# Optimization experiments

Measured on AMD Instinct MI355X. Metric: run time of the kernel, lower is better.

Reference implementation:

```python
import jax, jax.numpy as jnp
import numpy as np

# dims
B, L, D = 2, 2048, 768
K, KQ, M = 12, 6, 4          # heads, query heads, thetas
H = D // K                    # 64 head dim (expand_factor=1)
NREP = K // KQ                # 2
MEM = K * H                   # 768
FLAT = K * H * M              # 3072
EXP = H * 3                   # 192 (out_expand_factor=3)
DSW = EXP * 2                 # 384 swiglu per head
LAT = D // 4                  # 192
CK = 4                        # conv kernel size
TH_MIN, TH_MAX = 1e-3, 3.0


def setup_inputs() -> dict:
    key = jax.random.key(0)
    ks = jax.random.split(key, 10)
    rn = lambda k, sh, s=0.02: jax.random.normal(k, sh, jnp.float32) * s
    # faithful parameter inits from the flax module
    grid_m = np.geomspace(TH_MIN, TH_MAX, M)
    theta_d_raw = jnp.asarray(
        np.log(np.exp(np.tile(grid_m.reshape(1, 1, 1, 1, M), (1, 1, K, H, 1))) - 1.0 + 1e-4),
        jnp.float32)
    decay_slopes = jnp.asarray(np.log(np.exp(np.geomspace(1e-3, 0.1, K)) - 1.0), jnp.float32)
    return {
        "x": jax.random.normal(ks[0], (B, L, D), jnp.float32),
        "W_mem": rn(ks[1], (D, MEM + K)),
        "conv_k": rn(ks[2], (CK, 1, MEM + K), 0.2),
        "W_q": rn(ks[3], (D, KQ * H * M * 2)),
        "theta_d_raw": theta_d_raw,
        "decay_slopes": decay_slopes,
        "score_scale": jnp.ones((K,), jnp.float32),
        "tanh_scale": jnp.ones((K,), jnp.float32),
        "W_re": rn(ks[4], (K, H, DSW), 0.05),
        "W_im": rn(ks[5], (K, H, DSW), 0.05),
        "norm_scale": jnp.ones((1, 1, K, H), jnp.float32),
        "gate_W": jnp.zeros((D, K), jnp.float32),
        "gate_b": jnp.full((K,), -3.0, jnp.float32),
        "skip_down_W": rn(ks[6], (D, LAT)),
        "skip_up_W": rn(ks[7], (LAT, K * DSW)),
        "highway_scale": jnp.ones((1, 1, K, 1), jnp.float32),
        "out_W": rn(ks[8], (K * EXP, D)),
    }


def reference(x, W_mem, conv_k, W_q, theta_d_raw, decay_slopes, score_scale, tanh_scale,
              W_re, W_im, norm_scale, gate_W, gate_b, skip_down_W, skip_up_W,
              highway_scale, out_W):
    b, l, _ = x.shape
    # memory stream: dense proj + depthwise causal conv
    z = x @ W_mem                                                     # (b,l,MEM+K)
    z = jax.lax.conv_general_dilated(z, conv_k, (1,), [(CK - 1, 0)],
                                     dimension_numbers=('NWC', 'WIO', 'NWC'),
                                     feature_group_count=MEM + K)
    k_val = z[..., :MEM].reshape(b, l, K, H)
    s_raw = z[..., MEM:].reshape(b, l, K, 1)
    q = (x @ W_q).reshape(b, l, KQ, H, M, 2)
    q_re, q_im = q[..., 0], q[..., 1]
    # multi-frequency theta grid + trapezoid quadrature weights
    theta_d = jax.nn.softplus(theta_d_raw) + 1e-4
    ta = jnp.cumsum(theta_d, axis=-1)
    total = ta[..., -1:]
    rng = TH_MAX - TH_MIN
    theta = TH_MIN + ta / total * rng                                 # (1,1,K,H,M)
    dth = (ta[..., 1:] - ta[..., :-1]) * (rng / total)
    w_int = jnp.concatenate([dth[..., :1] * 0.5,
                             0.5 * (dth[..., :-1] + dth[..., 1:]),
                             dth[..., -1:] * 0.5], axis=-1)           # (1,1,K,H,M)
    # ALiBi-like decay anchored at sequence end (all decay heads)
    pos = jnp.arange(l, dtype=jnp.float32)
    slopes = jax.nn.softplus(decay_slopes).reshape(1, 1, K, 1)
    dist = jnp.maximum(jnp.float32(l - 1) - pos, 0.0)
    log_tw = -slopes * dist[None, :, None, None]                      # (1,l,K,1)
    log_p = jnp.clip(score_scale[None, None, :, None] * s_raw, -20.0, 20.0)
    p_w = jnp.exp(log_p + log_tw)                                     # (b,l,K,1)
    # complex rotation of keys by per-head/per-freq phase
    kvw = k_val[..., None] * p_w[..., None]                           # (b,l,K,H,1)
    phi = jnp.tanh(tanh_scale.reshape(1, 1, K, 1, 1) * k_val[..., None]) * theta  # (b,l,K,H,M)
    re_k = kvw * jnp.cos(phi)
    im_k = kvw * jnp.sin(phi)
    # fused prefix-sum over time of (denominator, Re, Im)
    merged = jnp.concatenate([p_w[..., 0],
                              re_k.reshape(b, l, FLAT),
                              im_k.reshape(b, l, FLAT)], axis=-1)
    cs = jnp.cumsum(merged, axis=1)
    den, num_re, num_im = cs[..., :K], cs[..., K:K + FLAT], cs[..., K + FLAT:]
    inv_den = 1.0 / jnp.maximum(den[..., None], 1e-4)                 # (b,l,K,1)
    s_re = (num_re.reshape(b, l, K, H, M) * inv_den[..., None]).reshape(b, l, KQ, NREP, H, M)
    s_im = (num_im.reshape(b, l, K, H, M) * inv_den[..., None]).reshape(b, l, KQ, NREP, H, M)
    w_g = w_int.reshape(1, 1, KQ, NREP, H, M)
    qr, qi = q_re[:, :, :, None], q_im[:, :, :, None]                 # GQA broadcast over n_rep
    out_re = jnp.sum((s_re * qr + s_im * qi) * w_g, axis=-1).reshape(b, l, K, H)
    out_im = jnp.sum((s_im * qr - s_re * qi) * w_g, axis=-1).reshape(b, l, K, H)
    # gated spectral output + low-rank highway skip, swiglu, out proj
    gate = jax.nn.sigmoid(x @ gate_W + gate_b)[..., None]             # (b,l,K,1)
    y_re = jnp.einsum('blkh,khn->blkn', out_re * norm_scale, W_re)
    y_im = jnp.einsum('blkh,khn->blkn', out_im * norm_scale, W_im)
    y_spec = (y_re + y_im) * gate                                     # (b,l,K,DSW)
    y_dir = ((x @ skip_down_W) @ skip_up_W).reshape(b, l, K, DSW)
    yv_s, yg_s = jnp.split(y_spec, 2, axis=-1)
    yv_d, yg_d = jnp.split(y_dir, 2, axis=-1)
    y_val = yv_s + yv_d * highway_scale
    y_gate = yg_s + yg_d * highway_scale
    y = (y_val * jax.nn.silu(y_gate)).reshape(b, l, K * EXP)
    return y @ out_W
```

## Files before the change

kernel.cpp:

```cpp
#include <hip/hip_runtime.h>
#include <math.h>

#define B_    2
#define L_    2048
#define D_    768
#define K_    12
#define KQ_   6
#define M_    4
#define H_    64
#define ZC_   780
#define NTOK_ 4096
#define NC_   64
#define LC_   32
#define QST_  3072
#define XPN_  4096
#define ZOFF_ 3276

typedef __attribute__((ext_vector_type(8))) _Float16 half8;
typedef __attribute__((ext_vector_type(4))) float f32x4;

__device__ __forceinline__ float softplus_f(float x) {
  return (x > 20.f) ? x : log1pf(expf(x));
}

__device__ __forceinline__ float fast_tanh(float x) {
  float xx = fminf(fmaxf(x, -10.f), 10.f);
  float e = __expf(2.f * xx);
  return (e - 1.f) / (e + 1.f);
}

__device__ __forceinline__ void async16(const _Float16* g, _Float16* l) {
  __builtin_amdgcn_global_load_lds(
      (const __attribute__((address_space(1))) unsigned int*)g,
      (__attribute__((address_space(3))) unsigned int*)l, 16, 0, 0);
}

__device__ __forceinline__ int permcol(int n) {
  int isg = (n >= 192) ? 1 : 0;
  int j = n - 192 * isg;
  return (j >> 4) * 32 + (isg << 4) + (j & 15);
}

#define FENCE() asm volatile("" ::: "memory")

__device__ __forceinline__ void cvt_t_body(float (*tile)[33], int bx, int by, int kz,
                                           const float* src, long sKs, int srs,
                                           _Float16* dh, long dKs, int dst, int doff,
                                           int R, int Nact, int Nst, bool perm, float scale) {
  const float* s = src + (size_t)kz * sKs;
  _Float16* dhh = dh + (size_t)kz * dKs;
  const int kb = bx * 32;
  const int nb = by * 32;
  const int tx = threadIdx.x & 31, ty = threadIdx.x >> 5;
  for (int i = ty; i < 32; i += 8) {
    int kk = kb + i, n = nb + tx;
    tile[i][tx] = (kk < R && n < Nact) ? s[(size_t)kk * srs + n] : 0.f;
  }
  __syncthreads();
  for (int i = ty; i < 32; i += 8) {
    int n = nb + i, kk = kb + tx;
    if (kk < R && n < Nst) {
      float v = tile[tx][i] * scale;
      int dn = perm ? permcol(n) : n;
      dhh[(size_t)dn * dst + doff + kk] = (_Float16)v;
    }
  }
}

__global__ __launch_bounds__(256)
void prep_kernel(const float* __restrict__ x,
                 const float* __restrict__ W_mem, const float* __restrict__ W_q,
                 const float* __restrict__ skip_down_W, const float* __restrict__ out_W,
                 const float* __restrict__ W_re, const float* __restrict__ W_im,
                 const float* __restrict__ skip_up_W, const float* __restrict__ hs,
                 const float* __restrict__ gate_W,
                 const float* __restrict__ theta_d_raw, const float* __restrict__ decay,
                 _Float16* __restrict__ x_h,
                 _Float16* __restrict__ xpb_h, _Float16* __restrict__ outw_h,
                 _Float16* __restrict__ bsp_h,
                 float* __restrict__ theta_tab, float* __restrict__ w_tab,
                 float* __restrict__ slopes_sp) {
  __shared__ float tile[32][33];
  int b = blockIdx.x;
  if (b < 3) {
    int idx = b * 256 + threadIdx.x;
    if (idx < K_) slopes_sp[idx] = softplus_f(decay[idx]);
    if (idx >= K_ * H_) return;
    float td[M_], ta[M_];
#pragma unroll
    for (int m = 0; m < M_; ++m) td[m] = softplus_f(theta_d_raw[idx * M_ + m]) + 1e-4f;
    ta[0] = td[0];
#pragma unroll
    for (int m = 1; m < M_; ++m) ta[m] = ta[m - 1] + td[m];
    float total = ta[M_ - 1];
    float rs = 2.999f / total;
#pragma unroll
    for (int m = 0; m < M_; ++m) theta_tab[idx * M_ + m] = 0.001f + ta[m] * rs;
    float d0 = (ta[1] - ta[0]) * rs;
    float d1 = (ta[2] - ta[1]) * rs;
    float d2 = (ta[3] - ta[2]) * rs;
    w_tab[idx * M_ + 0] = 0.5f * d0;
    w_tab[idx * M_ + 1] = 0.5f * (d0 + d1);
    w_tab[idx * M_ + 2] = 0.5f * (d1 + d2);
    w_tab[idx * M_ + 3] = 0.5f * d2;
    return;
  }
  b -= 3;
  if (b < 6360) {
    if (b < 672) {
      cvt_t_body(tile, b % 24, b / 24, 0, W_mem, 0, ZC_, xpb_h + (size_t)ZOFF_ * 768,
                 0, 768, 0, 768, ZC_, ZC_, false, 1.f);
      return;
    }
    b -= 672;
    if (b < 2304) {
      cvt_t_body(tile, b % 24, b / 24, 0, W_q, 0, 3072, xpb_h, 0, 768, 0, 768,
                 3072, 3072, false, 1.f);
      return;
    }
    b -= 2304;
    if (b < 192) {
      cvt_t_body(tile, b % 24, b / 24, 0, skip_down_W, 0, 192, xpb_h + (size_t)3072 * 768,
                 0, 768, 0, 768, 192, 192, false, 1.f);
      return;
    }
    b -= 192;
    if (b < 1728) {
      cvt_t_body(tile, b % 72, b / 72, 0, out_W, 0, 768, outw_h, 0, 2304, 0, 2304,
                 768, 768, false, 1.f);
      return;
    }
    b -= 1728;
    if (b < 288) {
      cvt_t_body(tile, b % 2, (b / 2) % 12, b / 24, W_re, 64L * 384, 384, bsp_h,
                 384L * 320, 320, 0, 64, 384, 384, true, 1.f);
      return;
    }
    b -= 288;
    if (b < 288) {
      cvt_t_body(tile, b % 2, (b / 2) % 12, b / 24, W_im, 64L * 384, 384, bsp_h,
                 384L * 320, 320, 64, 64, 384, 384, true, 1.f);
      return;
    }
    b -= 288;
    if (b < 864) {
      int kz = b / 72;
      cvt_t_body(tile, b % 6, (b / 6) % 12, kz, skip_up_W, 384, 4608, bsp_h,
                 384L * 320, 320, 128, 192, 384, 384, true, hs[kz]);
      return;
    }
    b -= 864;
    cvt_t_body(tile, b, 0, 0, gate_W, 0, K_, xpb_h + (size_t)3264 * 768,
               0, 768, 0, 768, K_, K_, false, 1.f);
    return;
  }
  b -= 6360;
  size_t i = (size_t)b * 256 + threadIdx.x;
  if (i < (size_t)NTOK_ * D_) {
    x_h[i] = (_Float16)x[i];
  }
}

__global__ __launch_bounds__(512, 2)
void xproj256_kernel(const _Float16* __restrict__ Ah, const _Float16* __restrict__ Bh,
                     float* __restrict__ C, _Float16* __restrict__ YH,
                     _Float16* __restrict__ QH, float* __restrict__ GL) {
  __shared__ __align__(16) _Float16 sA[2][2][2][128][32];
  __shared__ __align__(16) _Float16 sB[2][2][2][128][32];

  const int bid = blockIdx.x;
  const int xcd = bid & 7, s = bid >> 3;
  const int by = xcd * 2 + (s & 1);
  const int bx = s >> 1;
  const int bm0 = by * 256, bn0 = bx * 256;

  const int tid = threadIdx.x;
  const int lane = tid & 63;
  const int wave = tid >> 6;
  const int m16 = lane & 15, quad = lane >> 4;
  const int wr = wave >> 2;
  const int wc = wave & 3;
  const int bhalf = wc >> 1;
  const int brow0 = (wc & 1) * 64;

  f32x4 acc[8][4];
#pragma unroll
  for (int i = 0; i < 8; ++i)
#pragma unroll
    for (int j = 0; j < 4; ++j) acc[i][j] = (f32x4){0.f, 0.f, 0.f, 0.f};

  const int sr = tid >> 2;
  const int lb = tid & 3;
  const int ssw = (sr >> 1) & 3;

  auto stageA = [&](int t, int h) {
    const int bb = t & 1;
    const _Float16* g = Ah + (size_t)(bm0 + h * 128 + sr) * 768 + t * 64
                        + ((lb ^ ssw) << 3);
    async16(g,      &sA[bb][h][0][0][0] + (size_t)tid * 8);
    async16(g + 32, &sA[bb][h][1][0][0] + (size_t)tid * 8);
  };
  auto stageB = [&](int t, int h) {
    const int bb = t & 1;
    const _Float16* g = Bh + (size_t)(bn0 + h * 128 + sr) * 768 + t * 64
                        + ((lb ^ ssw) << 3);
    async16(g,      &sB[bb][h][0][0][0] + (size_t)tid * 8);
    async16(g + 32, &sB[bb][h][1][0][0] + (size_t)tid * 8);
  };

  auto ldA = [&](int bb, int r, int kk) -> half8 {
    return *(const half8*)&sA[bb][wr][kk][r][(quad ^ ((r >> 1) & 3)) << 3];
  };
  auto ldB = [&](int bb, int r, int kk) -> half8 {
    return *(const half8*)&sB[bb][bhalf][kk][r][(quad ^ ((r >> 1) & 3)) << 3];
  };

  half8 aLo[8], aHi[8], bLo[4], bHi[4];

  stageB(0, 0); stageB(0, 1); stageA(0, 0); stageA(0, 1);
  stageB(1, 0); stageB(1, 1); stageA(1, 0); stageA(1, 1);
  __builtin_amdgcn_s_waitcnt(0x0F78);
  FENCE(); __builtin_amdgcn_s_barrier(); FENCE();
#pragma unroll
  for (int m = 0; m < 4; ++m)
#pragma unroll
    for (int kk = 0; kk < 2; ++kk) aLo[m * 2 + kk] = ldA(0, m * 16 + m16, kk);
#pragma unroll
  for (int n = 0; n < 2; ++n)
#pragma unroll
    for (int kk = 0; kk < 2; ++kk) bLo[n * 2 + kk] = ldB(0, brow0 + n * 16 + m16, kk);

  for (int t = 0; t < 12; ++t) {
    const int bb = t & 1;
    const int nb = bb ^ 1;
#pragma unroll
    for (int n = 0; n < 2; ++n)
#pragma unroll
      for (int kk = 0; kk < 2; ++kk)
        bHi[n * 2 + kk] = ldB(bb, brow0 + (n + 2) * 16 + m16, kk);
#pragma unroll
    for (int m = 0; m < 4; ++m)
#pragma unroll
      for (int kk = 0; kk < 2; ++kk)
        aHi[m * 2 + kk] = ldA(bb, 64 + m * 16 + m16, kk);
    FENCE(); __builtin_amdgcn_s_barrier(); FENCE();
    if (t < 10) { stageB(t + 2, 0); stageB(t + 2, 1); stageA(t + 2, 0); stageA(t + 2, 1); }
    FENCE();
    if (t < 10)
      __builtin_amdgcn_s_waitcnt(0x0F78);
    else
      __builtin_amdgcn_s_waitcnt(0x0F70);
    FENCE(); __builtin_amdgcn_s_barrier(); FENCE();
    __builtin_amdgcn_s_setprio(1);
#pragma unroll
    for (int kk = 0; kk < 2; ++kk)
#pragma unroll
      for (int m = 0; m < 4; ++m)
#pragma unroll
        for (int n = 0; n < 2; ++n)
          acc[m][n] = __builtin_amdgcn_mfma_f32_16x16x32_f16(aLo[m * 2 + kk], bLo[n * 2 + kk],
                                                             acc[m][n], 0, 0, 0);
#pragma unroll
    for (int kk = 0; kk < 2; ++kk)
#pragma unroll
      for (int m = 0; m < 4; ++m)
#pragma unroll
        for (int n = 2; n < 4; ++n)
          acc[m][n] = __builtin_amdgcn_mfma_f32_16x16x32_f16(aLo[m * 2 + kk], bHi[(n - 2) * 2 + kk],
                                                             acc[m][n], 0, 0, 0);
    __builtin_amdgcn_s_setprio(0);
    if (t < 11) {
#pragma unroll
      for (int m = 0; m < 4; ++m)
#pragma unroll
        for (int kk = 0; kk < 2; ++kk)
          aLo[m * 2 + kk] = ldA(nb, m * 16 + m16, kk);
    }
    __builtin_amdgcn_s_setprio(1);
#pragma unroll
    for (int kk = 0; kk < 2; ++kk)
#pragma unroll
      for (int m = 0; m < 4; ++m)
#pragma unroll
        for (int n = 0; n < 2; ++n)
          acc[m + 4][n] = __builtin_amdgcn_mfma_f32_16x16x32_f16(aHi[m * 2 + kk], bLo[n * 2 + kk],
                                                                 acc[m + 4][n], 0, 0, 0);
    __builtin_amdgcn_s_setprio(0);
    if (t < 11) {
#pragma unroll
      for (int n = 0; n < 2; ++n)
#pragma unroll
        for (int kk = 0; kk < 2; ++kk)
          bLo[n * 2 + kk] = ldB(nb, brow0 + n * 16 + m16, kk);
    }
    __builtin_amdgcn_s_setprio(1);
#pragma unroll
    for (int kk = 0; kk < 2; ++kk)
#pragma unroll
      for (int m = 0; m < 4; ++m)
#pragma unroll
        for (int n = 2; n < 4; ++n)
          acc[m + 4][n] = __builtin_amdgcn_mfma_f32_16x16x32_f16(aHi[m * 2 + kk], bHi[(n - 2) * 2 + kk],
                                                                 acc[m + 4][n], 0, 0, 0);
    __builtin_amdgcn_s_setprio(0);
  }

#pragma unroll
  for (int m = 0; m < 8; ++m) {
    const int row0 = bm0 + wr * 128 + m * 16 + quad * 4;
#pragma unroll
    for (int n = 0; n < 4; ++n) {
      const int col = bn0 + wc * 64 + n * 16 + m16;
      if (col < 3072) {
#pragma unroll
        for (int r = 0; r < 4; ++r)
          QH[(size_t)(row0 + r) * QST_ + col] = (_Float16)acc[m][n][r];
      } else if (col < 3264) {
        const int jj = col - 3072;
#pragma unroll
        for (int r = 0; r < 4; ++r)
          YH[(size_t)(row0 + r) * 192 + jj] = (_Float16)acc[m][n][r];
      } else if (col < 3276) {
        const int kk = col - 3264;
#pragma unroll
        for (int r = 0; r < 4; ++r)
          GL[(size_t)(row0 + r) * K_ + kk] = acc[m][n][r];
      } else if (col < 3276 + ZC_) {
        const int wz = col - ZOFF_;
#pragma unroll
        for (int r = 0; r < 4; ++r)
          C[(size_t)(row0 + r) * ZC_ + wz] = acc[m][n][r];
      }
    }
  }
}

__global__ __launch_bounds__(512, 2)
void outproj256_kernel(const _Float16* __restrict__ Ah, const _Float16* __restrict__ Bh,
                       float* __restrict__ out, float* __restrict__ part) {
  __shared__ __align__(16) _Float16 sA[2][2][2][128][32];
  __shared__ __align__(16) _Float16 sB[2][2][2][128][32];

  const int bid = blockIdx.x;
  const int xcd = bid & 7, s = bid >> 3;
  const int g = xcd * 24 + s;
  const int by = g & 15;
  const int c = g >> 4;
  const int kz_ = c / 3, bx = c - kz_ * 3;
  const int bm0 = by * 256, bn0 = bx * 256;
  const int kt0 = kz_ * 9;

  const int tid = threadIdx.x;
  const int lane = tid & 63;
  const int wave = tid >> 6;
  const int m16 = lane & 15, quad = lane >> 4;
  const int wr = wave >> 2;
  const int wc = wave & 3;
  const int bhalf = wc >> 1;
  const int brow0 = (wc & 1) * 64;

  f32x4 acc[8][4];
#pragma unroll
  for (int i = 0; i < 8; ++i)
#pragma unroll
    for (int j = 0; j < 4; ++j) acc[i][j] = (f32x4){0.f, 0.f, 0.f, 0.f};

  const int sr = tid >> 2;
  const int lbk = tid & 3;
  const int ssw = (sr >> 1) & 3;

  auto stageA = [&](int lt, int h) {
    const int bb = lt & 1;
    const _Float16* gp = Ah + (size_t)(bm0 + h * 128 + sr) * 2304 + (kt0 + lt) * 64
                         + ((lbk ^ ssw) << 3);
    async16(gp,      &sA[bb][h][0][0][0] + (size_t)tid * 8);
    async16(gp + 32, &sA[bb][h][1][0][0] + (size_t)tid * 8);
  };
  auto stageB = [&](int lt, int h) {
    const int bb = lt & 1;
    const _Float16* gp = Bh + (size_t)(bn0 + h * 128 + sr) * 2304 + (kt0 + lt) * 64
                         + ((lbk ^ ssw) << 3);
    async16(gp,      &sB[bb][h][0][0][0] + (size_t)tid * 8);
    async16(gp + 32, &sB[bb][h][1][0][0] + (size_t)tid * 8);
  };

  auto ldA = [&](int bb, int r, int kk) -> half8 {
    return *(const half8*)&sA[bb][wr][kk][r][(quad ^ ((r >> 1) & 3)) << 3];
  };
  auto ldB = [&](int bb, int r, int kk) -> half8 {
    return *(const half8*)&sB[bb][bhalf][kk][r][(quad ^ ((r >> 1) & 3)) << 3];
  };

  half8 aLo[8], aHi[8], bLo[4], bHi[4];

  stageB(0, 0); stageB(0, 1); stageA(0, 0); stageA(0, 1);
  stageB(1, 0); stageB(1, 1); stageA(1, 0); stageA(1, 1);
  __builtin_amdgcn_s_waitcnt(0x0F78);
  FENCE(); __builtin_amdgcn_s_barrier(); FENCE();
#pragma unroll
  for (int m = 0; m < 4; ++m)
#pragma unroll
    for (int kk = 0; kk < 2; ++kk) aLo[m * 2 + kk] = ldA(0, m * 16 + m16, kk);
#pragma unroll
  for (int n = 0; n < 2; ++n)
#pragma unroll
    for (int kk = 0; kk < 2; ++kk) bLo[n * 2 + kk] = ldB(0, brow0 + n * 16 + m16, kk);

  for (int t = 0; t < 9; ++t) {
    const int bb = t & 1;
    const int nb = bb ^ 1;
#pragma unroll
    for (int n = 0; n < 2; ++n)
#pragma unroll
      for (int kk = 0; kk < 2; ++kk)
        bHi[n * 2 + kk] = ldB(bb, brow0 + (n + 2) * 16 + m16, kk);
#pragma unroll
    for (int m = 0; m < 4; ++m)
#pragma unroll
      for (int kk = 0; kk < 2; ++kk)
        aHi[m * 2 + kk] = ldA(bb, 64 + m * 16 + m16, kk);
    FENCE(); __builtin_amdgcn_s_barrier(); FENCE();
    if (t < 7) { stageB(t + 2, 0); stageB(t + 2, 1); stageA(t + 2, 0); stageA(t + 2, 1); }
    FENCE();
    if (t < 7)
      __builtin_amdgcn_s_waitcnt(0x0F78);
    else
      __builtin_amdgcn_s_waitcnt(0x0F70);
    FENCE(); __builtin_amdgcn_s_barrier(); FENCE();
    __builtin_amdgcn_s_setprio(1);
#pragma unroll
    for (int kk = 0; kk < 2; ++kk)
#pragma unroll
      for (int m = 0; m < 4; ++m)
#pragma unroll
        for (int n = 0; n < 2; ++n)
          acc[m][n] = __builtin_amdgcn_mfma_f32_16x16x32_f16(aLo[m * 2 + kk], bLo[n * 2 + kk],
                                                             acc[m][n], 0, 0, 0);
#pragma unroll
    for (int kk = 0; kk < 2; ++kk)
#pragma unroll
      for (int m = 0; m < 4; ++m)
#pragma unroll
        for (int n = 2; n < 4; ++n)
          acc[m][n] = __builtin_amdgcn_mfma_f32_16x16x32_f16(aLo[m * 2 + kk], bHi[(n - 2) * 2 + kk],
                                                             acc[m][n], 0, 0, 0);
    __builtin_amdgcn_s_setprio(0);
    if (t < 8) {
#pragma unroll
      for (int m = 0; m < 4; ++m)
#pragma unroll
        for (int kk = 0; kk < 2; ++kk)
          aLo[m * 2 + kk] = ldA(nb, m * 16 + m16, kk);
    }
    __builtin_amdgcn_s_setprio(1);
#pragma unroll
    for (int kk = 0; kk < 2; ++kk)
#pragma unroll
      for (int m = 0; m < 4; ++m)
#pragma unroll
        for (int n = 0; n < 2; ++n)
          acc[m + 4][n] = __builtin_amdgcn_mfma_f32_16x16x32_f16(aHi[m * 2 + kk], bLo[n * 2 + kk],
                                                                 acc[m + 4][n], 0, 0, 0);
    __builtin_amdgcn_s_setprio(0);
    if (t < 8) {
#pragma unroll
      for (int n = 0; n < 2; ++n)
#pragma unroll
        for (int kk = 0; kk < 2; ++kk)
          bLo[n * 2 + kk] = ldB(nb, brow0 + n * 16 + m16, kk);
    }
    __builtin_amdgcn_s_setprio(1);
#pragma unroll
    for (int kk = 0; kk < 2; ++kk)
#pragma unroll
      for (int m = 0; m < 4; ++m)
#pragma unroll
        for (int n = 2; n < 4; ++n)
          acc[m + 4][n] = __builtin_amdgcn_mfma_f32_16x16x32_f16(aHi[m * 2 + kk], bHi[(n - 2) * 2 + kk],
                                                                 acc[m + 4][n], 0, 0, 0);
    __builtin_amdgcn_s_setprio(0);
  }

  float* dst = (kz_ == 0) ? out : part + (size_t)(kz_ - 1) * NTOK_ * 768;
#pragma unroll
  for (int m = 0; m < 8; ++m) {
    const int row0 = bm0 + wr * 128 + m * 16 + quad * 4;
#pragma unroll
    for (int n = 0; n < 4; ++n) {
      const int col = bn0 + wc * 64 + n * 16 + m16;
#pragma unroll
      for (int r = 0; r < 4; ++r)
        dst[(size_t)(row0 + r) * 768 + col] = acc[m][n][r];
    }
  }
}

__global__ __launch_bounds__(256)
void redout_kernel(float* __restrict__ o, const float* __restrict__ p) {
  const size_t i = (size_t)blockIdx.x * 256 + threadIdx.x;
  const f32x4* pv = (const f32x4*)p;
  f32x4 v = ((const f32x4*)o)[i];
  v += pv[i];
  v += pv[i + 786432];
  v += pv[i + 2 * 786432];
  ((f32x4*)o)[i] = v;
}

__global__ __launch_bounds__(256)
void spec_gemm_kernel(const _Float16* __restrict__ Ah, const _Float16* __restrict__ Bh,
                      const _Float16* __restrict__ A2, _Float16* __restrict__ YH) {
  __shared__ __align__(16) _Float16 sA[2][128 * 32];
  __shared__ __align__(16) _Float16 sB[2][128 * 32];
  const int Kd = 320;
  int bid = blockIdx.x;
  int xcd = bid & 7, s = bid >> 3;
  int kz = s / 12;
  int w = s % 12;
  int bx = w % 3;
  int by = (xcd << 2) + w / 3;
  const _Float16* A0 = Ah + (size_t)kz * ((size_t)NTOK_ * 128);
  const _Float16* B0 = Bh + (size_t)kz * (384L * 320);
  const int bm0 = by * 128;
  const int bn0 = bx * 128;
  const int tid = threadIdx.x;
  const int wave = tid >> 6, lane = tid & 63;
  const int m16 = lane & 15, quad = lane >> 4;
  const int wr = (wave & 1) * 64, wc = (wave >> 1) * 64;

  f32x4 acc[4][4];
#pragma unroll
  for (int i = 0; i < 4; ++i)
#pragma unroll
    for (int j = 0; j < 4; ++j) acc[i][j] = (f32x4){0.f, 0.f, 0.f, 0.f};

  const int lin = tid * 8;
  const int lrow = lin >> 5;
  const int lblk = (lin >> 3) & 3;
  const int csw = ((lblk ^ ((lrow >> 1) & 3)) << 3);

  auto stage = [&](int k0, int kb) {
    if (k0 < 128) {
      const _Float16* gA = A0 + (size_t)(bm0 + lrow) * 128 + (k0 + csw);
      async16(gA, &sA[kb][lin]);
      async16(gA + (size_t)64 * 128, &sA[kb][lin + 2048]);
    } else {
      const _Float16* gA = A2 + (size_t)(bm0 + lrow) * 192 + (k0 - 128 + csw);
      async16(gA, &sA[kb][lin]);
      async16(gA + (size_t)64 * 192, &sA[kb][lin + 2048]);
    }
    const _Float16* gB = B0 + (size_t)(bn0 + lrow) * Kd + (k0 + csw);
    async16(gB, &sB[kb][lin]);
    async16(gB + (size_t)64 * Kd, &sB[kb][lin + 2048]);
  };

  const int niter = Kd / 32;
  stage(0, 0);
  stage(32, 1);

  for (int it = 0; it < niter; ++it) {
    if (it == niter - 1)
      __builtin_amdgcn_s_waitcnt(0x0F70);
    else
      __builtin_amdgcn_s_waitcnt(0x0F74);
    __builtin_amdgcn_s_barrier();
    asm volatile("" ::: "memory");
    const int kb = it & 1;
    half8 a0[4], b0[4];
#pragma unroll
    for (int i = 0; i < 4; ++i) {
      const int rA = wr + i * 16 + m16;
      a0[i] = *(const half8*)&sA[kb][rA * 32 + ((quad ^ ((rA >> 1) & 3)) << 3)];
    }
#pragma unroll
    for (int j = 0; j < 4; ++j) {
      const int rB = wc + j * 16 + m16;
      b0[j] = *(const half8*)&sB[kb][rB * 32 + ((quad ^ ((rB >> 1) & 3)) << 3)];
    }
#pragma unroll
    for (int i = 0; i < 4; ++i)
#pragma unroll
      for (int j = 0; j < 4; ++j)
        acc[i][j] = __builtin_amdgcn_mfma_f32_16x16x32_f16(a0[i], b0[j], acc[i][j], 0, 0, 0);
    asm volatile("" ::: "memory");
    __builtin_amdgcn_s_barrier();
    asm volatile("" ::: "memory");
    if (it + 2 < niter) stage((it + 2) * 32, kb);
  }

#pragma unroll
  for (int i = 0; i < 4; ++i) {
    const int row0 = bm0 + wr + i * 16 + quad * 4;
#pragma unroll
    for (int j = 0; j < 4; j += 2) {
      const int colv = bn0 + wc + j * 16 + m16;
      const int jout = (colv >> 5) * 16 + m16;
#pragma unroll
      for (int r = 0; r < 4; ++r) {
        float val = acc[i][j][r];
        float gg = acc[i][j + 1][r];
        float sg = gg / (1.f + __expf(-gg));
        YH[(size_t)(row0 + r) * 2304 + kz * 192 + jout] = (_Float16)(val * sg);
      }
    }
  }
}

__global__ __launch_bounds__(256)
void pass_a_kernel(const float* __restrict__ zp,
                   const float* __restrict__ ck,
                   const float* __restrict__ theta_tab,
                   const float* __restrict__ score_scale,
                   const float* __restrict__ tanh_scale,
                   const float* __restrict__ slopes_sp,
                   float* __restrict__ csums) {
  const int c = blockIdx.x, k = blockIdx.y, b = blockIdx.z;
  const int tid = threadIdx.x;
  const int m = tid & 3, h = tid >> 2;
  const int l0 = c * LC_;
  const size_t base = (((size_t)b * K_ + k) * NC_ + c) * 513;

  __shared__ float s_pw[LC_];
  __shared__ float s_kv[LC_][H_];
  __shared__ float s_th[LC_][H_];

  if (tid < 32) {
    const int chs = 768 + k;
    const float ss = score_scale[k], slope = slopes_sp[k];
    float cks[4];
#pragma unroll
    for (int w = 0; w < 4; ++w) cks[w] = ck[w * ZC_ + chs];
    float sraw = 0.f;
#pragma unroll
    for (int j = 0; j < 4; ++j) {
      int lp_ = l0 + tid - 3 + j;
      float zs = (lp_ >= 0) ? zp[((size_t)b * L_ + lp_) * ZC_ + chs] : 0.f;
      sraw += zs * cks[j];
    }
    float lp = fminf(fmaxf(ss * sraw, -20.f), 20.f);
    int l = l0 + tid;
    float pw = __expf(lp - slope * (float)(L_ - 1 - l));
    s_pw[tid] = pw;
    float tot = pw;
    tot += __shfl_xor(tot, 1);
    tot += __shfl_xor(tot, 2);
    tot += __shfl_xor(tot, 4);
    tot += __shfl_xor(tot, 8);
    tot += __shfl_xor(tot, 16);
    if (tid == 0) csums[base] = tot;
  }

  {
    const int hh = tid >> 2, g = tid & 3;
    const int chkh = k * H_ + hh;
    const float ts = tanh_scale[k];
    float ckv[4];
#pragma unroll
    for (int w = 0; w < 4; ++w) ckv[w] = ck[w * ZC_ + chkh];
    const int lbase = l0 + g * 8;
    float z3 = 0.f, z2 = 0.f, z1 = 0.f;
#pragma unroll
    for (int p = 0; p < 3; ++p) {
      int lp_ = lbase - 3 + p;
      if (lp_ >= 0) {
        float z = zp[((size_t)b * L_ + lp_) * ZC_ + chkh];
        if (p == 0) z3 = z; else if (p == 1) z2 = z; else z1 = z;
      }
    }
#pragma unroll
    for (int j = 0; j < 8; ++j) {
      float z0 = zp[((size_t)b * L_ + lbase + j) * ZC_ + chkh];
      float kv = z3 * ckv[0] + z2 * ckv[1] + z1 * ckv[2] + z0 * ckv[3];
      z3 = z2; z2 = z1; z1 = z0;
      s_kv[g * 8 + j][hh] = kv;
      s_th[g * 8 + j][hh] = fast_tanh(ts * kv);
    }
  }
  __syncthreads();

  const int chk = k * H_ + h;
  const float theta_v = theta_tab[chk * M_ + m];
  float sre = 0.f, sim = 0.f;
#pragma unroll 8
  for (int ll = 0; ll < LC_; ++ll) {
    float kvp = s_kv[ll][h] * s_pw[ll];
    float ph = s_th[ll][h] * theta_v;
    sre += kvp * __cosf(ph);
    sim += kvp * __sinf(ph);
  }
  csums[base + 1 + h * 4 + m] = sre;
  csums[base + 1 + 256 + h * 4 + m] = sim;
}

__global__ void pass_b_kernel(const float* __restrict__ csums,
                              float* __restrict__ cpre) {
  int bk = blockIdx.y;
  int comp = blockIdx.x * 64 + threadIdx.x;
  if (comp >= 513) return;
  float run = 0.f;
  size_t base = (size_t)bk * NC_ * 513 + comp;
#pragma unroll 4
  for (int c = 0; c < NC_; ++c) {
    cpre[base + (size_t)c * 513] = run;
    run += csums[base + (size_t)c * 513];
  }
}

__global__ __launch_bounds__(256)
void pass_c_kernel(const float* __restrict__ zp,
                   const float* __restrict__ ck,
                   const _Float16* __restrict__ qh,
                   const float* __restrict__ theta_tab,
                   const float* __restrict__ w_tab,
                   const float* __restrict__ score_scale,
                   const float* __restrict__ tanh_scale,
                   const float* __restrict__ slopes_sp,
                   const float* __restrict__ cpre,
                   const float* __restrict__ gatelin,
                   const float* __restrict__ gate_b,
                   const float* __restrict__ ns,
                   _Float16* __restrict__ asp) {
  const int c = blockIdx.x, k = blockIdx.y, b = blockIdx.z;
  const int tid = threadIdx.x;
  const int m = tid & 3, h = tid >> 2;
  const int l0 = c * LC_;
  const size_t base = (((size_t)b * K_ + k) * NC_ + c) * 513;

  __shared__ float s_pw[LC_];
  __shared__ float s_inv[LC_];
  __shared__ float s_sg[LC_];
  __shared__ float s_kv[LC_][H_];
  __shared__ float s_th[LC_][H_];

  if (tid < 32) {
    const int chs = 768 + k;
    const float ss = score_scale[k], slope = slopes_sp[k];
    const float gb = gate_b[k];
    float cks[4];
#pragma unroll
    for (int w = 0; w < 4; ++w) cks[w] = ck[w * ZC_ + chs];
    float sraw = 0.f;
#pragma unroll
    for (int j = 0; j < 4; ++j) {
      int lp_ = l0 + tid - 3 + j;
      float zs = (lp_ >= 0) ? zp[((size_t)b * L_ + lp_) * ZC_ + chs] : 0.f;
      sraw += zs * cks[j];
    }
    float lp = fminf(fmaxf(ss * sraw, -20.f), 20.f);
    int l = l0 + tid;
    float pw = __expf(lp - slope * (float)(L_ - 1 - l));
    s_pw[tid] = pw;
    float pref = pw;
#pragma unroll
    for (int off = 1; off < 32; off <<= 1) {
      float nv = __shfl_up(pref, off);
      if (tid >= off) pref += nv;
    }
    float den = cpre[base] + pref;
    s_inv[tid] = 1.f / fmaxf(den, 1e-4f);
    float gl = gatelin[((size_t)b * L_ + l) * K_ + k];
    s_sg[tid] = 1.f / (1.f + __expf(-(gl + gb)));
  }

  {
    const int hh = tid >> 2, g = tid & 3;
    const int chkh = k * H_ + hh;
    const float ts = tanh_scale[k];
    float ckv[4];
#pragma unroll
    for (int w = 0; w < 4; ++w) ckv[w] = ck[w * ZC_ + chkh];
    const int lbase = l0 + g * 8;
    float z3 = 0.f, z2 = 0.f, z1 = 0.f;
#pragma unroll
    for (int p = 0; p < 3; ++p) {
      int lp_ = lbase - 3 + p;
      if (lp_ >= 0) {
        float z = zp[((size_t)b * L_ + lp_) * ZC_ + chkh];
        if (p == 0) z3 = z; else if (p == 1) z2 = z; else z1 = z;
      }
    }
#pragma unroll
    for (int j = 0; j < 8; ++j) {
      float z0 = zp[((size_t)b * L_ + lbase + j) * ZC_ + chkh];
      float kv = z3 * ckv[0] + z2 * ckv[1] + z1 * ckv[2] + z0 * ckv[3];
      z3 = z2; z2 = z1; z1 = z0;
      s_kv[g * 8 + j][hh] = kv;
      s_th[g * 8 + j][hh] = fast_tanh(ts * kv);
    }
  }
  __syncthreads();

  const int chk = k * H_ + h;
  const float theta_v = theta_tab[chk * M_ + m];
  const float w = w_tab[chk * M_ + m];
  const float nsv = ns[chk];
  const int kq = k >> 1;
  const int qidx = ((kq * H_ + h) * M_ + m) * 2;
  float sre = cpre[base + 1 + h * 4 + m];
  float sim = cpre[base + 1 + 256 + h * 4 + m];
#pragma unroll 4
  for (int ll = 0; ll < LC_; ++ll) {
    float kvp = s_kv[ll][h] * s_pw[ll];
    float ph = s_th[ll][h] * theta_v;
    sre += kvp * __cosf(ph);
    sim += kvp * __sinf(ph);
    float inv = s_inv[ll];
    float s_re = sre * inv, s_im = sim * inv;
    size_t t = (size_t)b * L_ + l0 + ll;
    size_t qb = t * QST_ + qidx;
    float qr = (float)qh[qb], qi = (float)qh[qb + 1];
    float tr = (s_re * qr + s_im * qi) * w;
    float ti = (s_im * qr - s_re * qi) * w;
    tr += __shfl_xor(tr, 1); tr += __shfl_xor(tr, 2);
    ti += __shfl_xor(ti, 1); ti += __shfl_xor(ti, 2);
    if (m == 0) {
      float g = s_sg[ll] * nsv;
      size_t ab = ((size_t)k * NTOK_ + t) * 128;
      asp[ab + h] = (_Float16)(tr * g);
      asp[ab + 64 + h] = (_Float16)(ti * g);
    }
  }
}

extern "C" void kernel_launch(void* const* d_in, const int* in_sizes, int n_in,
                              void* d_out, int out_size, void* d_ws, size_t ws_size,
                              hipStream_t stream) {
  const float* x            = (const float*)d_in[0];
  const float* W_mem        = (const float*)d_in[1];
  const float* conv_k       = (const float*)d_in[2];
  const float* W_q          = (const float*)d_in[3];
  const float* theta_d_raw  = (const float*)d_in[4];
  const float* decay_slopes = (const float*)d_in[5];
  const float* score_scale  = (const float*)d_in[6];
  const float* tanh_scale   = (const float*)d_in[7];
  const float* W_re         = (const float*)d_in[8];
  const float* W_im         = (const float*)d_in[9];
  const float* norm_scale   = (const float*)d_in[10];
  const float* gate_W       = (const float*)d_in[11];
  const float* gate_b       = (const float*)d_in[12];
  const float* skip_down_W  = (const float*)d_in[13];
  const float* skip_up_W    = (const float*)d_in[14];
  const float* highway_scale= (const float*)d_in[15];
  const float* out_W        = (const float*)d_in[16];
  float* out = (float*)d_out;
  float* ws = (float*)d_ws;

  float* theta_tab = ws;
  float* w_tab     = theta_tab + 3072;
  float* slopes_sp = w_tab + 3072;
  float* z_pre     = slopes_sp + 16;
  float* gatelin   = z_pre + (size_t)NTOK_ * ZC_;
  float* csums     = gatelin + (size_t)NTOK_ * K_;
  float* cpre      = csums + (size_t)B_ * K_ * NC_ * 513;
  _Float16* q_h    = (_Float16*)(cpre + (size_t)B_ * K_ * NC_ * 513);
  _Float16* y_h    = q_h + (size_t)NTOK_ * QST_;
  float* f32_end   = (float*)(y_h + (size_t)NTOK_ * 2304);

  float* part = z_pre;

  _Float16* fp = (_Float16*)f32_end;
  _Float16* x_h    = fp;                fp += (size_t)NTOK_ * D_;
  _Float16* xpb_h  = fp;                fp += (size_t)XPN_ * 768;
  _Float16* outw_h = fp;                fp += (size_t)768 * 2304;
  _Float16* asp2_h = fp;                fp += (size_t)K_ * NTOK_ * 128;
  _Float16* bsp_h  = fp;                fp += (size_t)K_ * 384 * 320;
  _Float16* lat_h  = fp;                fp += (size_t)NTOK_ * 192;

  prep_kernel<<<18651, 256, 0, stream>>>(x, W_mem, W_q, skip_down_W, out_W, W_re, W_im,
                                         skip_up_W, highway_scale, gate_W,
                                         theta_d_raw, decay_slopes,
                                         x_h, xpb_h, outw_h, bsp_h,
                                         theta_tab, w_tab, slopes_sp);

  xproj256_kernel<<<256, 512, 0, stream>>>(x_h, xpb_h, z_pre, lat_h, q_h, gatelin);

  pass_a_kernel<<<dim3(NC_, K_, B_), 256, 0, stream>>>(z_pre, conv_k, theta_tab, score_scale,
                                                       tanh_scale, slopes_sp, csums);
  pass_b_kernel<<<dim3(9, B_ * K_), 64, 0, stream>>>(csums, cpre);
  pass_c_kernel<<<dim3(NC_, K_, B_), 256, 0, stream>>>(z_pre, conv_k, q_h, theta_tab, w_tab,
                                                       score_scale, tanh_scale, slopes_sp, cpre,
                                                       gatelin, gate_b, norm_scale, asp2_h);

  spec_gemm_kernel<<<1152, 256, 0, stream>>>(asp2_h, bsp_h, lat_h, y_h);

  outproj256_kernel<<<192, 512, 0, stream>>>(y_h, outw_h, out, part);
  redout_kernel<<<3072, 256, 0, stream>>>(out, part);
}
```

Measured before the change: 253.0 us.

## Retile x-projection GEMM to 256x128 blocks with 32-wide K steps

Replaces the 256x256-tile projection GEMM with a 256x128 tile, K-step of 32, fewer accumulators per wave and launch bounds allowing four blocks per CU, doubling the grid to 512 blocks. It aims to raise occupancy and fill more CUs, since the old 256-block grid may underfill the device. In exchange each block reuses less data per load, so global and LDS traffic rise and there are twice as many loop iterations and barriers.

```diff
diff --git a/kernel.cpp b/kernel.cpp
--- a/kernel.cpp
+++ b/kernel.cpp
@@ -161,153 +161,106 @@
   }
 }
 
-__global__ __launch_bounds__(512, 2)
-void xproj256_kernel(const _Float16* __restrict__ Ah, const _Float16* __restrict__ Bh,
-                     float* __restrict__ C, _Float16* __restrict__ YH,
-                     _Float16* __restrict__ QH, float* __restrict__ GL) {
-  __shared__ __align__(16) _Float16 sA[2][2][2][128][32];
-  __shared__ __align__(16) _Float16 sB[2][2][2][128][32];
+__global__ __launch_bounds__(512, 4)
+void xprojk_kernel(const _Float16* __restrict__ Ah, const _Float16* __restrict__ Bh,
+                   float* __restrict__ C, _Float16* __restrict__ YH,
+                   _Float16* __restrict__ QH, float* __restrict__ GL) {
+  __shared__ __align__(16) _Float16 sA[2][2][128][32];
+  __shared__ __align__(16) _Float16 sB[2][128][32];
 
   const int bid = blockIdx.x;
   const int xcd = bid & 7, s = bid >> 3;
   const int by = xcd * 2 + (s & 1);
   const int bx = s >> 1;
-  const int bm0 = by * 256, bn0 = bx * 256;
+  const int bm0 = by * 256, bn0 = bx * 128;
 
   const int tid = threadIdx.x;
   const int lane = tid & 63;
   const int wave = tid >> 6;
   const int m16 = lane & 15, quad = lane >> 4;
-  const int wr = wave >> 2;
-  const int wc = wave & 3;
-  const int bhalf = wc >> 1;
-  const int brow0 = (wc & 1) * 64;
-
-  f32x4 acc[8][4];
-#pragma unroll
-  for (int i = 0; i < 8; ++i)
+  const int wr = wave >> 1;
+  const int wc = wave & 1;
+
+  f32x4 acc[4][4];
+#pragma unroll
+  for (int i = 0; i < 4; ++i)
 #pragma unroll
     for (int j = 0; j < 4; ++j) acc[i][j] = (f32x4){0.f, 0.f, 0.f, 0.f};
 
-  const int sr = tid >> 2;
+  const int sr4 = tid >> 2;
   const int lb = tid & 3;
-  const int ssw = (sr >> 1) & 3;
-
-  auto stageA = [&](int t, int h) {
+  const int ssw = (sr4 >> 1) & 3;
+
+  auto stageA = [&](int t) {
     const int bb = t & 1;
-    const _Float16* g = Ah + (size_t)(bm0 + h * 128 + sr) * 768 + t * 64
-                        + ((lb ^ ssw) << 3);
-    async16(g,      &sA[bb][h][0][0][0] + (size_t)tid * 8);
-    async16(g + 32, &sA[bb][h][1][0][0] + (size_t)tid * 8);
+    const _Float16* g = Ah + (size_t)(bm0 + sr4) * 768 + t * 32 + ((lb ^ ssw) << 3);
+    async16(g,                     &sA[bb][0][0][0] + (size_t)tid * 8);
+    async16(g + (size_t)128 * 768, &sA[bb][1][0][0] + (size_t)tid * 8);
   };
-  auto stageB = [&](int t, int h) {
+  auto stageB = [&](int t) {
     const int bb = t & 1;
-    const _Float16* g = Bh + (size_t)(bn0 + h * 128 + sr) * 768 + t * 64
-                        + ((lb ^ ssw) << 3);
-    async16(g,      &sB[bb][h][0][0][0] + (size_t)tid * 8);
-    async16(g + 32, &sB[bb][h][1][0][0] + (size_t)tid * 8);
+    const _Float16* g = Bh + (size_t)(bn0 + sr4) * 768 + t * 32 + ((lb ^ ssw) << 3);
+    async16(g, &sB[bb][0][0] + (size_t)tid * 8);
   };
 
-  auto ldA = [&](int bb, int r, int kk) -> half8 {
-    return *(const half8*)&sA[bb][wr][kk][r][(quad ^ ((r >> 1) & 3)) << 3];
+  auto ldA = [&](int bb, int r) -> half8 {
+    return *(const half8*)&sA[bb][r >> 7][r & 127][(quad ^ ((r >> 1) & 3)) << 3];
   };
-  auto ldB = [&](int bb, int r, int kk) -> half8 {
-    return *(const half8*)&sB[bb][bhalf][kk][r][(quad ^ ((r >> 1) & 3)) << 3];
+  auto ldB = [&](int bb, int r) -> half8 {
+    return *(const half8*)&sB[bb][r][(quad ^ ((r >> 1) & 3)) << 3];
   };
 
-  half8 aLo[8], aHi[8], bLo[4], bHi[4];
-
-  stageB(0, 0); stageB(0, 1); stageA(0, 0); stageA(0, 1);
-  stageB(1, 0); stageB(1, 1); stageA(1, 0); stageA(1, 1);
-  __builtin_amdgcn_s_waitcnt(0x0F78);
+  half8 a[4], b[4];
+
+  stageB(0); stageA(0);
+  stageB(1); stageA(1);
+  __builtin_amdgcn_s_waitcnt(0x0F73);
   FENCE(); __builtin_amdgcn_s_barrier(); FENCE();
 #pragma unroll
-  for (int m = 0; m < 4; ++m)
-#pragma unroll
-    for (int kk = 0; kk < 2; ++kk) aLo[m * 2 + kk] = ldA(0, m * 16 + m16, kk);
-#pragma unroll
-  for (int n = 0; n < 2; ++n)
-#pragma unroll
-    for (int kk = 0; kk < 2; ++kk) bLo[n * 2 + kk] = ldB(0, brow0 + n * 16 + m16, kk);
-
-  for (int t = 0; t < 12; ++t) {
+  for (int m = 0; m < 4; ++m) a[m] = ldA(0, wr * 64 + m * 16 + m16);
+#pragma unroll
+  for (int n = 0; n < 4; ++n) b[n] = ldB(0, wc * 64 + n * 16 + m16);
+
+  for (int t = 0; t < 24; ++t) {
     const int bb = t & 1;
     const int nb = bb ^ 1;
-#pragma unroll
-    for (int n = 0; n < 2; ++n)
-#pragma unroll
-      for (int kk = 0; kk < 2; ++kk)
-        bHi[n * 2 + kk] = ldB(bb, brow0 + (n + 2) * 16 + m16, kk);
-#pragma unroll
-    for (int m = 0; m < 4; ++m)
-#pragma unroll
-      for (int kk = 0; kk < 2; ++kk)
-        aHi[m * 2 + kk] = ldA(bb, 64 + m * 16 + m16, kk);
     FENCE(); __builtin_amdgcn_s_barrier(); FENCE();
-    if (t < 10) { stageB(t + 2, 0); stageB(t + 2, 1); stageA(t + 2, 0); stageA(t + 2, 1); }
+    if (t < 22) { stageB(t + 2); stageA(t + 2); }
     FENCE();
-    if (t < 10)
-      __builtin_amdgcn_s_waitcnt(0x0F78);
+    if (t < 22)
+      __builtin_amdgcn_s_waitcnt(0x0F73);
     else
       __builtin_amdgcn_s_waitcnt(0x0F70);
     FENCE(); __builtin_amdgcn_s_barrier(); FENCE();
     __builtin_amdgcn_s_setprio(1);
 #pragma unroll
-    for (int kk = 0; kk < 2; ++kk)
-#pragma unroll
-      for (int m = 0; m < 4; ++m)
-#pragma unroll
-        for (int n = 0; n < 2; ++n)
-          acc[m][n] = __builtin_amdgcn_mfma_f32_16x16x32_f16(aLo[m * 2 + kk], bLo[n * 2 + kk],
-                                                             acc[m][n], 0, 0, 0);
-#pragma unroll
-    for (int kk = 0; kk < 2; ++kk)
-#pragma unroll
-      for (int m = 0; m < 4; ++m)
-#pragma unroll
-        for (int n = 2; n < 4; ++n)
-          acc[m][n] = __builtin_amdgcn_mfma_f32_16x16x32_f16(aLo[m * 2 + kk], bHi[(n - 2) * 2 + kk],
-                                                             acc[m][n], 0, 0, 0);
+    for (int m = 0; m < 4; ++m)
+#pragma unroll
+      for (int n = 0; n < 2; ++n)
+        acc[m][n] = __builtin_amdgcn_mfma_f32_16x16x32_f16(a[m], b[n], acc[m][n], 0, 0, 0);
     __builtin_amdgcn_s_setprio(0);
-    if (t < 11) {
-#pragma unroll
-      for (int m = 0; m < 4; ++m)
-#pragma unroll
-        for (int kk = 0; kk < 2; ++kk)
-          aLo[m * 2 + kk] = ldA(nb, m * 16 + m16, kk);
+    if (t < 23) {
+#pragma unroll
+      for (int n = 0; n < 2; ++n) b[n] = ldB(nb, wc * 64 + n * 16 + m16);
     }
     __builtin_amdgcn_s_setprio(1);
 #pragma unroll
-    for (int kk = 0; kk < 2; ++kk)
-#pragma unroll
-      for (int m = 0; m < 4; ++m)
-#pragma unroll
-        for (int n = 0; n < 2; ++n)
-          acc[m + 4][n] = __builtin_amdgcn_mfma_f32_16x16x32_f16(aHi[m * 2 + kk], bLo[n * 2 + kk],
-                                                                 acc[m + 4][n], 0, 0, 0);
+    for (int m = 0; m < 4; ++m)
+#pragma unroll
+      for (int n = 2; n < 4; ++n)
+        acc[m][n] = __builtin_amdgcn_mfma_f32_16x16x32_f16(a[m], b[n], acc[m][n], 0, 0, 0);
     __builtin_amdgcn_s_setprio(0);
-    if (t < 11) {
-#pragma unroll
-      for (int n = 0; n < 2; ++n)
-#pragma unroll
-        for (int kk = 0; kk < 2; ++kk)
-          bLo[n * 2 + kk] = ldB(nb, brow0 + n * 16 + m16, kk);
-    }
-    __builtin_amdgcn_s_setprio(1);
-#pragma unroll
-    for (int kk = 0; kk < 2; ++kk)
-#pragma unroll
-      for (int m = 0; m < 4; ++m)
-#pragma unroll
-        for (int n = 2; n < 4; ++n)
-          acc[m + 4][n] = __builtin_amdgcn_mfma_f32_16x16x32_f16(aHi[m * 2 + kk], bHi[(n - 2) * 2 + kk],
-                                                                 acc[m + 4][n], 0, 0, 0);
-    __builtin_amdgcn_s_setprio(0);
-  }
-
-#pragma unroll
-  for (int m = 0; m < 8; ++m) {
-    const int row0 = bm0 + wr * 128 + m * 16 + quad * 4;
+    if (t < 23) {
+#pragma unroll
+      for (int m = 0; m < 4; ++m) a[m] = ldA(nb, wr * 64 + m * 16 + m16);
+#pragma unroll
+      for (int n = 2; n < 4; ++n) b[n] = ldB(nb, wc * 64 + n * 16 + m16);
+    }
+  }
+
+#pragma unroll
+  for (int m = 0; m < 4; ++m) {
+    const int row0 = bm0 + wr * 64 + m * 16 + quad * 4;
 #pragma unroll
     for (int n = 0; n < 4; ++n) {
       const int col = bn0 + wc * 64 + n * 16 + m16;
@@ -871,7 +824,7 @@
                                          x_h, xpb_h, outw_h, bsp_h,
                                          theta_tab, w_tab, slopes_sp);
 
-  xproj256_kernel<<<256, 512, 0, stream>>>(x_h, xpb_h, z_pre, lat_h, q_h, gatelin);
+  xprojk_kernel<<<512, 512, 0, stream>>>(x_h, xpb_h, z_pre, lat_h, q_h, gatelin);
 
   pass_a_kernel<<<dim3(NC_, K_, B_), 256, 0, stream>>>(z_pre, conv_k, theta_tab, score_scale,
                                                        tanh_scale, slopes_sp, csums);
```

After: 249.3 us. No clear change (-1.5%).
